# Kernel tuning notes

Measured on AMD Instinct MI355X. Metric: run time of the kernel, lower is better.

Reference implementation:

```python
import jax, jax.numpy as jnp
import numpy as np

N = 50000        # nodes
E = 1600000      # edges
NDIM_IN = 64
HID = 128        # hardcoded hidden width of first SAGELayer in E-GraphSAGE
NDIM_OUT = 128
EDIM = 32
EMBEDIM = 128
NCLASS = 2       # bin=True


def setup_inputs() -> dict:
    key = jax.random.key(0)
    ks = jax.random.split(key, 12)
    g = lambda k, shape: jax.random.normal(k, shape, jnp.float32) / np.sqrt(np.float32(shape[0]))
    return {
        "nfeats": jax.random.normal(ks[0], (N, NDIM_IN), jnp.float32),
        "efeats": jax.random.normal(ks[1], (E, EDIM), jnp.float32),
        "src": jax.random.randint(ks[2], (E,), 0, N),
        "dst": jax.random.randint(ks[3], (E,), 0, N),
        # SAGE layer 1: W_msg [ndim_in+edim -> 128], W_apply [ndim_in+128 -> 128]
        "Wm1": g(ks[4], (NDIM_IN + EDIM, HID)), "bm1": jnp.zeros((HID,), jnp.float32),
        "Wa1": g(ks[5], (NDIM_IN + HID, HID)), "ba1": jnp.zeros((HID,), jnp.float32),
        # SAGE layer 2: W_msg [128+edim -> ndim_out], W_apply [128+ndim_out -> ndim_out]
        "Wm2": g(ks[6], (HID + EDIM, NDIM_OUT)), "bm2": jnp.zeros((NDIM_OUT,), jnp.float32),
        "Wa2": g(ks[7], (HID + NDIM_OUT, NDIM_OUT)), "ba2": jnp.zeros((NDIM_OUT,), jnp.float32),
        # MLPPredictorEmbed: [2*ndim_out -> embedim] -> relu -> [embedim -> 2]
        "W1": g(ks[8], (2 * NDIM_OUT, EMBEDIM)), "b1": jnp.zeros((EMBEDIM,), jnp.float32),
        "W2": g(ks[9], (EMBEDIM, NCLASS)), "b2": jnp.zeros((NCLASS,), jnp.float32),
    }


def _sage_layer(h, efeats, src, dst, Wm, bm, Wa, ba):
    # per-edge message: relu(W_msg([h_src || e]))  -> [E, dout]
    m = jax.nn.relu(jnp.concatenate([h[src], efeats], axis=-1) @ Wm + bm)
    # mean aggregation by destination node (0 for isolated nodes, like DGL fn.mean)
    s = jax.ops.segment_sum(m, dst, num_segments=N)
    cnt = jax.ops.segment_sum(jnp.ones((m.shape[0], 1), m.dtype), dst, num_segments=N)
    h_neigh = s / jnp.maximum(cnt, 1.0)
    # node update: relu(W_apply([h || h_neigh]))
    return jax.nn.relu(jnp.concatenate([h, h_neigh], axis=-1) @ Wa + ba)


def reference(nfeats, efeats, src, dst,
              Wm1, bm1, Wa1, ba1, Wm2, bm2, Wa2, ba2,
              W1, b1, W2, b2):
    h = _sage_layer(nfeats, efeats, src, dst, Wm1, bm1, Wa1, ba1)   # [N, 128]
    h = _sage_layer(h, efeats, src, dst, Wm2, bm2, Wa2, ba2)        # [N, ndim_out]
    # edge predictor: MLP on [h_u || h_v] per edge
    z = jnp.concatenate([h[src], h[dst]], axis=-1)                   # [E, 2*ndim_out]
    score = jax.nn.relu(z @ W1 + b1) @ W2 + b2                       # [E, 2]
    return score
```

## Files before the change

### kernel.cpp

```cpp
#include <hip/hip_runtime.h>

#define N_NODES 50000
#define N_EDGES 1600000

typedef _Float16 h8 __attribute__((ext_vector_type(8)));
typedef float f4 __attribute__((ext_vector_type(4)));

__device__ inline h8 ld_h8(const _Float16* p) { return *(const h8*)p; }

__device__ inline h8 cvt2h8(f4 a, f4 b) {
    h8 r;
    r[0] = (_Float16)a[0]; r[1] = (_Float16)a[1]; r[2] = (_Float16)a[2]; r[3] = (_Float16)a[3];
    r[4] = (_Float16)b[0]; r[5] = (_Float16)b[1]; r[6] = (_Float16)b[2]; r[7] = (_Float16)b[3];
    return r;
}


__global__ void prep_weights(const float* __restrict__ Wm1, const float* __restrict__ Wa1,
                             const float* __restrict__ Wm2, const float* __restrict__ Wa2,
                             const float* __restrict__ W1,
                             _Float16* __restrict__ Wm1t, _Float16* __restrict__ Wa1t,
                             _Float16* __restrict__ Wm2t, _Float16* __restrict__ Wa2t,
                             _Float16* __restrict__ W1t)
{
    int i = blockIdx.x * 256 + threadIdx.x;
    if (i < 12288) {
        int o = i / 96, k = i % 96;
        int ks = k >> 5, q = (k >> 3) & 3, j = k & 7;
        int c = q ^ ((o >> 1) & 3);
        Wm1t[(ks * 128 + o) * 32 + c * 8 + j] = (_Float16)Wm1[k * 128 + o];
    } else if (i < 36864) {
        int jj = i - 12288; int o = jj / 192, k = jj % 192;
        Wa1t[o * 200 + k] = (_Float16)Wa1[k * 128 + o];
    } else if (i < 57344) {
        int jj = i - 36864; int o = jj / 160, k = jj % 160;
        int ks = k >> 5, q = (k >> 3) & 3, j = k & 7;
        int c = q ^ ((o >> 1) & 3);
        Wm2t[(ks * 128 + o) * 32 + c * 8 + j] = (_Float16)Wm2[k * 128 + o];
    } else if (i < 90112) {
        int jj = i - 57344; int o = jj >> 8, k = jj & 255;
        Wa2t[(o << 8) + k] = (_Float16)Wa2[k * 128 + o];
    } else if (i < 122880) {
        int jj = i - 90112; int o = jj >> 8, k = jj & 255;
        W1t[(o << 8) + k] = (_Float16)W1[k * 128 + o];
    }
}

__global__ void cvt_nfeats(const float* __restrict__ nf, _Float16* __restrict__ nf16)
{
    int i = blockIdx.x * 256 + threadIdx.x;
    nf16[i] = (_Float16)nf[i];
}


__global__ void hist_kernel(const int* __restrict__ dst, int* __restrict__ cnt)
{
    int e = blockIdx.x * 256 + threadIdx.x;
    atomicAdd(cnt + dst[e], 1);
}

__global__ void scan1_kernel(const int* __restrict__ cnt, int* __restrict__ tmp,
                             int* __restrict__ bsum)
{
    __shared__ int sh[256];
    int t = threadIdx.x, i = blockIdx.x * 256 + t;
    int v = (i < N_NODES) ? cnt[i] : 0;
    sh[t] = v; __syncthreads();
    for (int off = 1; off < 256; off <<= 1) {
        int x = (t >= off) ? sh[t - off] : 0;
        __syncthreads();
        sh[t] += x;
        __syncthreads();
    }
    if (i < N_NODES) tmp[i] = sh[t];
    if (t == 255) bsum[blockIdx.x] = sh[255];
}

__global__ void scan2_kernel(const int* __restrict__ bsum, int* __restrict__ bbase)
{
    __shared__ int sh[256];
    int t = threadIdx.x;
    int v = (t < 196) ? bsum[t] : 0;
    sh[t] = v; __syncthreads();
    for (int off = 1; off < 256; off <<= 1) {
        int x = (t >= off) ? sh[t - off] : 0;
        __syncthreads();
        sh[t] += x;
        __syncthreads();
    }
    if (t < 196) bbase[t] = sh[t] - v;
}

__global__ void scan3_kernel(const int* __restrict__ cnt, const int* __restrict__ tmp,
                             const int* __restrict__ bbase, int* __restrict__ cursor)
{
    int t = threadIdx.x, b = blockIdx.x, i = b * 256 + t;
    if (i < N_NODES) cursor[i] = tmp[i] - cnt[i] + bbase[b];
}

__global__ void scatter_kernel(const int* __restrict__ src, const int* __restrict__ dst,
                               int* __restrict__ cursor,
                               int2* __restrict__ pairs, int* __restrict__ dsts)
{
    int e = blockIdx.x * 256 + threadIdx.x;
    int d = dst[e];
    int pos = atomicAdd(cursor + d, 1);
    pairs[pos] = make_int2(e, src[e]);
    dsts[pos] = d;
}

__global__ void scatter_kernel_ef(const int* __restrict__ src, const int* __restrict__ dst,
                                  const float* __restrict__ efeats,
                                  int* __restrict__ cursor,
                                  int2* __restrict__ pairs, int* __restrict__ dsts,
                                  _Float16* __restrict__ efs)
{
    int e = blockIdx.x * 256 + threadIdx.x;
    int d = dst[e];
    const float* er = efeats + (size_t)e * 32;
    f4 v0 = *(const f4*)(er + 0),  v1 = *(const f4*)(er + 4);
    f4 v2 = *(const f4*)(er + 8),  v3 = *(const f4*)(er + 12);
    f4 v4 = *(const f4*)(er + 16), v5 = *(const f4*)(er + 20);
    f4 v6 = *(const f4*)(er + 24), v7 = *(const f4*)(er + 28);
    int pos = atomicAdd(cursor + d, 1);
    pairs[pos] = make_int2(e, src[e]);
    dsts[pos] = d;
    _Float16* ew = efs + (size_t)pos * 32;
    *(h8*)(ew + 0)  = cvt2h8(v0, v1);
    *(h8*)(ew + 8)  = cvt2h8(v2, v3);
    *(h8*)(ew + 16) = cvt2h8(v4, v5);
    *(h8*)(ew + 24) = cvt2h8(v6, v7);
}

template<int KSRC_H, int MINW, bool EF16>
__launch_bounds__(256, MINW)
__global__ void msg_kernel_sorted(const _Float16* __restrict__ ntab,
                                  const float* __restrict__ efeats,
                                  const _Float16* __restrict__ efs,
                                  const int2* __restrict__ pairs,
                                  const int* __restrict__ dsts,
                                  const _Float16* __restrict__ Wt,
                                  const float* __restrict__ bias,
                                  float* __restrict__ sacc)
{
    constexpr int EFSTEP = KSRC_H / 32;
    constexpr int KSTEPS = EFSTEP + 1;
    constexpr int BH = (KSRC_H + 32) * 128;
    constexpr int BBYTES = BH * 2;
    constexpr int SCRBYTES = 4 * 8 * 132 * 4;
    constexpr int LDSBYTES = BBYTES > SCRBYTES ? BBYTES : SCRBYTES;
    __shared__ __align__(16) char smem[LDSBYTES];
    _Float16* Bsh = (_Float16*)smem;

    const int tid = threadIdx.x;
    const int wave = tid >> 6, lane = tid & 63;
    const int q = lane >> 4, l15 = lane & 15;
    const int wbase = blockIdx.x * 128 + wave * 32;

    const int2 p0 = pairs[wbase + l15];
    const int2 p1 = pairs[wbase + 16 + l15];
    const int4 dv0 = *(const int4*)(dsts + wbase + q * 4);
    const int4 dv1 = *(const int4*)(dsts + wbase + 16 + q * 4);
    float bv[8];
#pragma unroll
    for (int nt = 0; nt < 8; nt++) bv[nt] = bias[nt * 16 + l15];

    const _Float16* r0 = ntab + (size_t)p0.y * KSRC_H + q * 8;
    const _Float16* r1 = ntab + (size_t)p1.y * KSRC_H + q * 8;
    h8 aA[EFSTEP], aB[EFSTEP];
#pragma unroll
    for (int ks = 0; ks < EFSTEP; ks++) {
        aA[ks] = ld_h8(r0 + ks * 32);
        aB[ks] = ld_h8(r1 + ks * 32);
    }
    h8 ef0h, ef1h;
    f4 e0a, e0b, e1a, e1b;
    if constexpr (EF16) {
        ef0h = ld_h8(efs + (size_t)(wbase + l15) * 32 + q * 8);
        ef1h = ld_h8(efs + (size_t)(wbase + 16 + l15) * 32 + q * 8);
    } else {
        const float* ep0 = efeats + (size_t)p0.x * 32 + q * 8;
        const float* ep1 = efeats + (size_t)p1.x * 32 + q * 8;
        e0a = *(const f4*)ep0; e0b = *(const f4*)(ep0 + 4);
        e1a = *(const f4*)ep1; e1b = *(const f4*)(ep1 + 4);
    }

    {
        const uint4* s4 = (const uint4*)Wt;
        uint4* d4 = (uint4*)smem;
        constexpr int n4 = BH / 8;
        for (int i = tid; i < n4; i += 256) d4[i] = s4[i];
    }
    __syncthreads();

    f4 acc[2][8];
#pragma unroll
    for (int t = 0; t < 2; t++)
#pragma unroll
        for (int nt = 0; nt < 8; nt++) acc[t][nt] = (f4){0.f, 0.f, 0.f, 0.f};

    const _Float16* bp = Bsh + l15 * 32 + ((q ^ ((l15 >> 1) & 3)) << 3);
#pragma unroll
    for (int ks = 0; ks < KSTEPS; ks++) {
        h8 a0, a1;
        if (ks < EFSTEP) {
            a0 = aA[ks]; a1 = aB[ks];
        } else {
            if constexpr (EF16) { a0 = ef0h; a1 = ef1h; }
            else { a0 = cvt2h8(e0a, e0b); a1 = cvt2h8(e1a, e1b); }
        }
#pragma unroll
        for (int nt = 0; nt < 8; nt++) {
            h8 b = ld_h8(bp + ks * 4096 + nt * 512);
            acc[0][nt] = __builtin_amdgcn_mfma_f32_16x16x32_f16(a0, b, acc[0][nt], 0, 0, 0);
            acc[1][nt] = __builtin_amdgcn_mfma_f32_16x16x32_f16(a1, b, acc[1][nt], 0, 0, 0);
        }
    }

    __syncthreads();

    float* wsch = (float*)smem + wave * 1056;

    const int df0 = __shfl(dv0.x, 0, 64);
    const int dl0 = __shfl(dv0.w, 48, 64);
    const int df1 = __shfl(dv1.x, 0, 64);
    const int dl1 = __shfl(dv1.w, 48, 64);

    auto unif16 = [&](const f4 (&a)[8], int d) {
        float sv[8];
#pragma unroll
        for (int nt = 0; nt < 8; nt++) {
            float s = fmaxf(a[nt][0] + bv[nt], 0.f) + fmaxf(a[nt][1] + bv[nt], 0.f)
                    + fmaxf(a[nt][2] + bv[nt], 0.f) + fmaxf(a[nt][3] + bv[nt], 0.f);
            s += __shfl_xor(s, 16, 64);
            s += __shfl_xor(s, 32, 64);
            sv[nt] = s;
        }
#pragma unroll
        for (int i = 0; i < 2; i++) {
            float x = (q == 0) ? sv[i*4] : (q == 1) ? sv[i*4+1] : (q == 2) ? sv[i*4+2] : sv[i*4+3];
            atomicAdd(sacc + (size_t)d * 128 + i * 64 + lane, x);
        }
    };

    auto scan16 = [&](const f4 (&a)[8], const int4 dv, int dfirst) {
        int dp = dfirst;
        float s0 = 0.f, s1 = 0.f;
#pragma unroll
        for (int h = 0; h < 2; h++) {
            if ((q >> 1) == h) {
                const int rloc = (q & 1) * 4;
#pragma unroll
                for (int nt = 0; nt < 8; nt++)
#pragma unroll
                    for (int r = 0; r < 4; r++)
                        wsch[(rloc + r) * 132 + nt * 16 + l15] = fmaxf(a[nt][r] + bv[nt], 0.f);
            }
            asm volatile("s_waitcnt lgkmcnt(0)" ::: "memory");
#pragma unroll
            for (int rr = 0; rr < 8; rr++) {
                const int rg = h * 8 + rr;
                const int sl = (rg >> 2) << 4;
                const int c = rg & 3;
                const int d = (c == 0) ? __shfl(dv.x, sl, 64)
                            : (c == 1) ? __shfl(dv.y, sl, 64)
                            : (c == 2) ? __shfl(dv.z, sl, 64)
                            :            __shfl(dv.w, sl, 64);
                const float v0 = wsch[rr * 132 + lane];
                const float v1 = wsch[rr * 132 + 64 + lane];
                if (d != dp) {
                    atomicAdd(sacc + (size_t)dp * 128 + lane, s0);
                    atomicAdd(sacc + (size_t)dp * 128 + 64 + lane, s1);
                    s0 = v0; s1 = v1; dp = d;
                } else {
                    s0 += v0; s1 += v1;
                }
            }
        }
        atomicAdd(sacc + (size_t)dp * 128 + lane, s0);
        atomicAdd(sacc + (size_t)dp * 128 + 64 + lane, s1);
    };

    if (df0 == dl1) {
        float sv[8];
#pragma unroll
        for (int nt = 0; nt < 8; nt++) {
            float s = fmaxf(acc[0][nt][0] + bv[nt], 0.f) + fmaxf(acc[0][nt][1] + bv[nt], 0.f)
                    + fmaxf(acc[0][nt][2] + bv[nt], 0.f) + fmaxf(acc[0][nt][3] + bv[nt], 0.f)
                    + fmaxf(acc[1][nt][0] + bv[nt], 0.f) + fmaxf(acc[1][nt][1] + bv[nt], 0.f)
                    + fmaxf(acc[1][nt][2] + bv[nt], 0.f) + fmaxf(acc[1][nt][3] + bv[nt], 0.f);
            s += __shfl_xor(s, 16, 64);
            s += __shfl_xor(s, 32, 64);
            sv[nt] = s;
        }
#pragma unroll
        for (int i = 0; i < 2; i++) {
            float x = (q == 0) ? sv[i*4] : (q == 1) ? sv[i*4+1] : (q == 2) ? sv[i*4+2] : sv[i*4+3];
            atomicAdd(sacc + (size_t)df0 * 128 + i * 64 + lane, x);
        }
    } else {
        if (df0 == dl0) unif16(acc[0], df0); else scan16(acc[0], dv0, df0);
        if (df1 == dl1) unif16(acc[1], df1); else scan16(acc[1], dv1, df1);
    }
}

template<int KSRC_H, bool SWIZ, int KPAD>
__launch_bounds__(256)
__global__ void apply_kernel(const _Float16* __restrict__ ntab,
                             const float* __restrict__ sacc,
                             const int* __restrict__ cnt,
                             const _Float16* __restrict__ Wt,
                             const float* __restrict__ bias,
                             _Float16* __restrict__ outtab)
{
    constexpr int KSTEPS = (KSRC_H + 128) / 32;
    __shared__ __align__(16) _Float16 Bsh[128 * KPAD];

    const int tid = threadIdx.x;
    if (SWIZ) {
        const uint4* s4 = (const uint4*)Wt;
        uint4* d4 = (uint4*)Bsh;
        for (int i = tid; i < 4096; i += 256) {
            int n = i >> 5, c = i & 31;
            d4[(n << 5) | (c ^ (n & 31))] = s4[i];
        }
    } else {
        const uint4* s4 = (const uint4*)Wt;
        uint4* d4 = (uint4*)Bsh;
        constexpr int n4 = 128 * KPAD / 8;
        for (int i = tid; i < n4; i += 256) d4[i] = s4[i];
    }
    __syncthreads();

    const int wave = tid >> 6, lane = tid & 63;
    const int q = lane >> 4, l15 = lane & 15;
    const int nbase = blockIdx.x * 128 + wave * 32;

    const int n0 = nbase + l15, n1 = nbase + 16 + l15;
    const int n0c = min(n0, N_NODES - 1), n1c = min(n1, N_NODES - 1);
    const _Float16* r0 = ntab + (size_t)n0c * KSRC_H;
    const _Float16* r1 = ntab + (size_t)n1c * KSRC_H;
    const float rcp0 = 1.0f / fmaxf((float)cnt[n0c], 1.0f);
    const float rcp1 = 1.0f / fmaxf((float)cnt[n1c], 1.0f);

    f4 acc[2][8];
#pragma unroll
    for (int t = 0; t < 2; t++)
#pragma unroll
        for (int nt = 0; nt < 8; nt++) acc[t][nt] = (f4){0.f, 0.f, 0.f, 0.f};

#pragma unroll
    for (int ks = 0; ks < KSTEPS; ks++) {
        h8 a0, a1;
        if (ks < KSRC_H / 32) {
            a0 = ld_h8(r0 + ks * 32 + q * 8);
            a1 = ld_h8(r1 + ks * 32 + q * 8);
        } else {
            const int kk = ks * 32 - KSRC_H + q * 8;
            const float* p0 = sacc + (size_t)n0c * 128 + kk;
            const float* p1 = sacc + (size_t)n1c * 128 + kk;
            f4 u0 = *(const f4*)p0 * rcp0, v0 = *(const f4*)(p0 + 4) * rcp0;
            f4 u1 = *(const f4*)p1 * rcp1, v1 = *(const f4*)(p1 + 4) * rcp1;
            a0 = cvt2h8(u0, v0);
            a1 = cvt2h8(u1, v1);
        }
#pragma unroll
        for (int nt = 0; nt < 8; nt++) {
            h8 b;
            if (SWIZ) {
                const int nrow = nt * 16 + l15;
                const int chunk = ((ks << 2) | q) ^ (nrow & 31);
                b = ld_h8(Bsh + (((nrow << 5) | chunk) << 3));
            } else {
                b = ld_h8(&Bsh[(nt * 16 + l15) * KPAD + ks * 32 + q * 8]);
            }
            acc[0][nt] = __builtin_amdgcn_mfma_f32_16x16x32_f16(a0, b, acc[0][nt], 0, 0, 0);
            acc[1][nt] = __builtin_amdgcn_mfma_f32_16x16x32_f16(a1, b, acc[1][nt], 0, 0, 0);
        }
    }

#pragma unroll
    for (int nt = 0; nt < 8; nt++) {
        const int col = nt * 16 + l15;
        const float bv = bias[col];
#pragma unroll
        for (int t = 0; t < 2; t++)
#pragma unroll
            for (int r = 0; r < 4; r++) {
                const int node = nbase + t * 16 + q * 4 + r;
                if (node < N_NODES) {
                    float v = fmaxf(acc[t][nt][r] + bv, 0.f);
                    outtab[(size_t)node * 128 + col] = (_Float16)v;
                }
            }
    }
}

__launch_bounds__(256)
__global__ void node_pq_kernel(const _Float16* __restrict__ h2,
                               const _Float16* __restrict__ W1t,
                               const float* __restrict__ b1,
                               _Float16* __restrict__ P,
                               float* __restrict__ Q)
{
    __shared__ __align__(16) _Float16 Bsh[128 * 256];

    const int tid = threadIdx.x;
    {
        const uint4* s4 = (const uint4*)W1t;
        uint4* d4 = (uint4*)Bsh;
        for (int i = tid; i < 4096; i += 256) {
            int n = i >> 5, c = i & 31;
            d4[(n << 5) | (c ^ (n & 31))] = s4[i];
        }
    }
    __syncthreads();

    const int wave = tid >> 6, lane = tid & 63;
    const int q = lane >> 4, l15 = lane & 15;
    const int nbase = blockIdx.x * 128 + wave * 32;

    const int n0 = nbase + l15, n1 = nbase + 16 + l15;
    const int n0c = min(n0, N_NODES - 1), n1c = min(n1, N_NODES - 1);
    const _Float16* r0 = h2 + (size_t)n0c * 128;
    const _Float16* r1 = h2 + (size_t)n1c * 128;

    f4 accP[2][8], accQ[2][8];
#pragma unroll
    for (int t = 0; t < 2; t++)
#pragma unroll
        for (int nt = 0; nt < 8; nt++) {
            accP[t][nt] = (f4){0.f, 0.f, 0.f, 0.f};
            accQ[t][nt] = (f4){0.f, 0.f, 0.f, 0.f};
        }

#pragma unroll
    for (int ks = 0; ks < 4; ks++) {
        h8 a0 = ld_h8(r0 + ks * 32 + q * 8);
        h8 a1 = ld_h8(r1 + ks * 32 + q * 8);
#pragma unroll
        for (int nt = 0; nt < 8; nt++) {
            const int nrow = nt * 16 + l15;
            const int cP = ((ks << 2) | q) ^ (nrow & 31);
            h8 bP = ld_h8(Bsh + (((nrow << 5) | cP) << 3));
            accP[0][nt] = __builtin_amdgcn_mfma_f32_16x16x32_f16(a0, bP, accP[0][nt], 0, 0, 0);
            accP[1][nt] = __builtin_amdgcn_mfma_f32_16x16x32_f16(a1, bP, accP[1][nt], 0, 0, 0);
            const int cQ = (((ks + 4) << 2) | q) ^ (nrow & 31);
            h8 bQ = ld_h8(Bsh + (((nrow << 5) | cQ) << 3));
            accQ[0][nt] = __builtin_amdgcn_mfma_f32_16x16x32_f16(a0, bQ, accQ[0][nt], 0, 0, 0);
            accQ[1][nt] = __builtin_amdgcn_mfma_f32_16x16x32_f16(a1, bQ, accQ[1][nt], 0, 0, 0);
        }
    }

#pragma unroll
    for (int nt = 0; nt < 8; nt++) {
        const int col = nt * 16 + l15;
        const float bq = b1[col];
#pragma unroll
        for (int t = 0; t < 2; t++)
#pragma unroll
            for (int r = 0; r < 4; r++) {
                const int node = nbase + t * 16 + q * 4 + r;
                if (node < N_NODES) {
                    P[(size_t)node * 128 + col] = (_Float16)accP[t][nt][r];
                    Q[(size_t)node * 128 + col] = accQ[t][nt][r] + bq;
                }
            }
    }
}

__launch_bounds__(256, 4)
__global__ void pred_elem_kernel(const _Float16* __restrict__ P,
                                 const float* __restrict__ Q,
                                 const int2* __restrict__ pairs,
                                 const int* __restrict__ dsts,
                                 const float* __restrict__ W2,
                                 const float* __restrict__ b2,
                                 float* __restrict__ out)
{
    __shared__ __align__(16) float w20sh[128];
    __shared__ __align__(16) float w21sh[128];

    const int tid = threadIdx.x;
    if (tid < 128) {
        w20sh[tid] = W2[tid * 2 + 0];
        w21sh[tid] = W2[tid * 2 + 1];
    }
    __syncthreads();

    const int slot = blockIdx.x * 256 + tid;
    const int2 pr = pairs[slot];
    const int d = dsts[slot];
    const _Float16* prow = P + (size_t)pr.y * 128;
    const float* qrow = Q + (size_t)d * 128;

    float o0 = 0.f, o1 = 0.f;
#pragma unroll
    for (int c = 0; c < 4; c++) {
        h8 pv[4];
#pragma unroll
        for (int i = 0; i < 4; i++) pv[i] = ld_h8(prow + c * 32 + i * 8);
        f4 qv[8];
#pragma unroll
        for (int i = 0; i < 8; i++) qv[i] = *(const f4*)(qrow + c * 32 + i * 4);
#pragma unroll
        for (int i = 0; i < 8; i++) {
            const f4 w0 = *(const f4*)(w20sh + c * 32 + i * 4);
            const f4 w1 = *(const f4*)(w21sh + c * 32 + i * 4);
#pragma unroll
            for (int j = 0; j < 4; j++) {
                const float pvf = (float)pv[i >> 1][(i & 1) * 4 + j];
                const float y = fmaxf(pvf + qv[i][j], 0.f);
                o0 += y * w0[j];
                o1 += y * w1[j];
            }
        }
    }

    out[(size_t)pr.x * 2 + 0] = o0 + b2[0];
    out[(size_t)pr.x * 2 + 1] = o1 + b2[1];
}

__launch_bounds__(256)
__global__ void pred_kernel(const _Float16* __restrict__ h2,
                            const int* __restrict__ src,
                            const int* __restrict__ dst,
                            const _Float16* __restrict__ W1t,
                            const float* __restrict__ b1,
                            const float* __restrict__ W2,
                            const float* __restrict__ b2,
                            float* __restrict__ out)
{
    __shared__ __align__(16) _Float16 Bsh[128 * 256];

    const int tid = threadIdx.x;
    {
        const uint4* s4 = (const uint4*)W1t;
        uint4* d4 = (uint4*)Bsh;
        for (int i = tid; i < 4096; i += 256) {
            int n = i >> 5, c = i & 31;
            d4[(n << 5) | (c ^ (n & 31))] = s4[i];
        }
    }
    __syncthreads();

    const int wave = tid >> 6, lane = tid & 63;
    const int q = lane >> 4, l15 = lane & 15;
    const int ebase = blockIdx.x * 128 + wave * 32;

    const int e0 = ebase + l15, e1 = ebase + 16 + l15;
    const _Float16* rs0 = h2 + (size_t)src[e0] * 128;
    const _Float16* rd0 = h2 + (size_t)dst[e0] * 128;
    const _Float16* rs1 = h2 + (size_t)src[e1] * 128;
    const _Float16* rd1 = h2 + (size_t)dst[e1] * 128;

    f4 acc[2][8];
#pragma unroll
    for (int t = 0; t < 2; t++)
#pragma unroll
        for (int nt = 0; nt < 8; nt++) acc[t][nt] = (f4){0.f, 0.f, 0.f, 0.f};

#pragma unroll
    for (int ks = 0; ks < 8; ks++) {
        h8 a0, a1;
        if (ks < 4) {
            a0 = ld_h8(rs0 + ks * 32 + q * 8);
            a1 = ld_h8(rs1 + ks * 32 + q * 8);
        } else {
            a0 = ld_h8(rd0 + (ks - 4) * 32 + q * 8);
            a1 = ld_h8(rd1 + (ks - 4) * 32 + q * 8);
        }
#pragma unroll
        for (int nt = 0; nt < 8; nt++) {
            const int nrow = nt * 16 + l15;
            const int chunk = ((ks << 2) | q) ^ (nrow & 31);
            h8 b = ld_h8(Bsh + (((nrow << 5) | chunk) << 3));
            acc[0][nt] = __builtin_amdgcn_mfma_f32_16x16x32_f16(a0, b, acc[0][nt], 0, 0, 0);
            acc[1][nt] = __builtin_amdgcn_mfma_f32_16x16x32_f16(a1, b, acc[1][nt], 0, 0, 0);
        }
    }

    float o[2][4][2];
#pragma unroll
    for (int t = 0; t < 2; t++)
#pragma unroll
        for (int r = 0; r < 4; r++) { o[t][r][0] = 0.f; o[t][r][1] = 0.f; }

#pragma unroll
    for (int nt = 0; nt < 8; nt++) {
        const int nrow = nt * 16 + l15;
        const float bv = b1[nrow];
        const float w20 = W2[nrow * 2 + 0];
        const float w21 = W2[nrow * 2 + 1];
#pragma unroll
        for (int t = 0; t < 2; t++)
#pragma unroll
            for (int r = 0; r < 4; r++) {
                float y = fmaxf(acc[t][nt][r] + bv, 0.f);
                o[t][r][0] += y * w20;
                o[t][r][1] += y * w21;
            }
    }

#pragma unroll
    for (int m = 1; m < 16; m <<= 1) {
#pragma unroll
        for (int t = 0; t < 2; t++)
#pragma unroll
            for (int r = 0; r < 4; r++) {
                o[t][r][0] += __shfl_xor(o[t][r][0], m, 64);
                o[t][r][1] += __shfl_xor(o[t][r][1], m, 64);
            }
    }

    if (l15 < 8) {
        const int r = l15 >> 1, c = l15 & 1;
        const float bb = c ? b2[1] : b2[0];
#pragma unroll
        for (int t = 0; t < 2; t++) {
            float v0 = (r == 0) ? o[t][0][0] : (r == 1) ? o[t][1][0] : (r == 2) ? o[t][2][0] : o[t][3][0];
            float v1 = (r == 0) ? o[t][0][1] : (r == 1) ? o[t][1][1] : (r == 2) ? o[t][2][1] : o[t][3][1];
            float v = (c ? v1 : v0) + bb;
            out[(size_t)(ebase + t * 16 + q * 4 + r) * 2 + c] = v;
        }
    }
}


extern "C" void kernel_launch(void* const* d_in, const int* in_sizes, int n_in,
                              void* d_out, int out_size, void* d_ws, size_t ws_size,
                              hipStream_t stream)
{
    const float* nfeats = (const float*)d_in[0];
    const float* efeats = (const float*)d_in[1];
    const int*   src    = (const int*)d_in[2];
    const int*   dst    = (const int*)d_in[3];
    const float* Wm1 = (const float*)d_in[4],  *bm1 = (const float*)d_in[5];
    const float* Wa1 = (const float*)d_in[6],  *ba1 = (const float*)d_in[7];
    const float* Wm2 = (const float*)d_in[8],  *bm2 = (const float*)d_in[9];
    const float* Wa2 = (const float*)d_in[10], *ba2 = (const float*)d_in[11];
    const float* W1  = (const float*)d_in[12], *b1  = (const float*)d_in[13];
    const float* W2  = (const float*)d_in[14], *b2  = (const float*)d_in[15];
    float* out = (float*)d_out;

    char* ws = (char*)d_ws;
    float*     s     = (float*)(ws);
    int*       cnt   = (int*)(ws + 25600000);
    int*       tmp   = (int*)(ws + 25800000);
    int*       cursor= (int*)(ws + 26000000);
    int*       bsum  = (int*)(ws + 26200000);
    int*       bbase = (int*)(ws + 26201024);
    _Float16*  nf16  = (_Float16*)(ws + 26202048);
    int2*      pairs = (int2*)(ws + 32602048);
    int*       dsts  = (int*)(ws + 45402048);
    _Float16*  h1    = (_Float16*)(ws + 51802048);
    _Float16*  Wm1t  = (_Float16*)(ws + 64602048);
    _Float16*  Wa1t  = (_Float16*)(ws + 64626624);
    _Float16*  Wm2t  = (_Float16*)(ws + 64677824);
    _Float16*  Wa2t  = (_Float16*)(ws + 64718784);
    _Float16*  W1t   = (_Float16*)(ws + 64784320);

    const bool big_ws  = ws_size >= (size_t)77800000;
    const bool ef16_ws = ws_size >= (size_t)180100000;
    _Float16* h2 = big_ws ? (_Float16*)(ws + 64849920)
                          : (_Float16*)(ws + 26202048);
    _Float16* efs16 = (_Float16*)(ws + 77649920);

    hipMemsetAsync(s, 0, 25600000, stream);
    hipMemsetAsync(cnt, 0, 200000, stream);

    prep_weights<<<480, 256, 0, stream>>>(Wm1, Wa1, Wm2, Wa2, W1, Wm1t, Wa1t, Wm2t, Wa2t, W1t);
    cvt_nfeats<<<12500, 256, 0, stream>>>(nfeats, nf16);

    hist_kernel<<<6250, 256, 0, stream>>>(dst, cnt);
    scan1_kernel<<<196, 256, 0, stream>>>(cnt, tmp, bsum);
    scan2_kernel<<<1, 256, 0, stream>>>(bsum, bbase);
    scan3_kernel<<<196, 256, 0, stream>>>(cnt, tmp, bbase, cursor);
    if (ef16_ws)
        scatter_kernel_ef<<<6250, 256, 0, stream>>>(src, dst, efeats, cursor, pairs, dsts, efs16);
    else
        scatter_kernel<<<6250, 256, 0, stream>>>(src, dst, cursor, pairs, dsts);

    if (ef16_ws)
        msg_kernel_sorted<64, 4, true><<<12500, 256, 0, stream>>>(nf16, efeats, efs16, pairs, dsts, Wm1t, bm1, s);
    else
        msg_kernel_sorted<64, 4, false><<<12500, 256, 0, stream>>>(nf16, efeats, nullptr, pairs, dsts, Wm1t, bm1, s);
    apply_kernel<64, false, 200><<<391, 256, 0, stream>>>(nf16, s, cnt, Wa1t, ba1, h1);

    hipMemsetAsync(s, 0, 25600000, stream);
    if (ef16_ws)
        msg_kernel_sorted<128, 4, true><<<12500, 256, 0, stream>>>(h1, efeats, efs16, pairs, dsts, Wm2t, bm2, s);
    else
        msg_kernel_sorted<128, 4, false><<<12500, 256, 0, stream>>>(h1, efeats, nullptr, pairs, dsts, Wm2t, bm2, s);
    apply_kernel<128, true, 256><<<391, 256, 0, stream>>>(h1, s, cnt, Wa2t, ba2, h2);

    if (big_ws) {
        _Float16* P = h1;
        float*    Q = s;
        node_pq_kernel<<<391, 256, 0, stream>>>(h2, W1t, b1, P, Q);
        pred_elem_kernel<<<6250, 256, 0, stream>>>(P, Q, pairs, dsts, W2, b2, out);
    } else {
        pred_kernel<<<12500, 256, 0, stream>>>(h2, src, dst, W1t, b1, W2, b2, out);
    }
}
```

Measured before the change: 1.027 ms.

## Make message kernels persistent to amortize per-block weight staging into LDS

Replaces the one-tile-per-block message kernels (12500 blocks of 256 threads) with a persistent kernel of 512 blocks of 512 threads, each looping over a contiguous range of 256-edge tiles. The weight matrix is copied into LDS once per block instead of once per 128 edges, cutting repeated global-to-LDS staging and barriers. The scatter scratch gets its own LDS region so no barrier is needed between tiles. The trade-offs are that gather-load latency is no longer hidden by many independent blocks, there is possible load imbalance across the fixed grid, and LDS per block grows, which can lower occupancy.

```diff
diff --git a/kernel.cpp b/kernel.cpp
--- a/kernel.cpp
+++ b/kernel.cpp
@@ -132,175 +132,177 @@
     *(h8*)(ew + 24) = cvt2h8(v6, v7);
 }
 
-template<int KSRC_H, int MINW, bool EF16>
-__launch_bounds__(256, MINW)
-__global__ void msg_kernel_sorted(const _Float16* __restrict__ ntab,
-                                  const float* __restrict__ efeats,
-                                  const _Float16* __restrict__ efs,
-                                  const int2* __restrict__ pairs,
-                                  const int* __restrict__ dsts,
-                                  const _Float16* __restrict__ Wt,
-                                  const float* __restrict__ bias,
-                                  float* __restrict__ sacc)
+template<int KSRC_H, bool EF16>
+__launch_bounds__(512, 4)
+__global__ void msg_kernel_ms(const _Float16* __restrict__ ntab,
+                              const float* __restrict__ efeats,
+                              const _Float16* __restrict__ efs,
+                              const int2* __restrict__ pairs,
+                              const int* __restrict__ dsts,
+                              const _Float16* __restrict__ Wt,
+                              const float* __restrict__ bias,
+                              float* __restrict__ sacc,
+                              int ntiles, int tpb)
 {
     constexpr int EFSTEP = KSRC_H / 32;
     constexpr int KSTEPS = EFSTEP + 1;
     constexpr int BH = (KSRC_H + 32) * 128;
     constexpr int BBYTES = BH * 2;
-    constexpr int SCRBYTES = 4 * 8 * 132 * 4;
-    constexpr int LDSBYTES = BBYTES > SCRBYTES ? BBYTES : SCRBYTES;
-    __shared__ __align__(16) char smem[LDSBYTES];
+    __shared__ __align__(16) char smem[BBYTES + 8 * 8 * 132 * 4];
+
     _Float16* Bsh = (_Float16*)smem;
-
     const int tid = threadIdx.x;
     const int wave = tid >> 6, lane = tid & 63;
     const int q = lane >> 4, l15 = lane & 15;
-    const int wbase = blockIdx.x * 128 + wave * 32;
-
-    const int2 p0 = pairs[wbase + l15];
-    const int2 p1 = pairs[wbase + 16 + l15];
-    const int4 dv0 = *(const int4*)(dsts + wbase + q * 4);
-    const int4 dv1 = *(const int4*)(dsts + wbase + 16 + q * 4);
-    float bv[8];
-#pragma unroll
-    for (int nt = 0; nt < 8; nt++) bv[nt] = bias[nt * 16 + l15];
-
-    const _Float16* r0 = ntab + (size_t)p0.y * KSRC_H + q * 8;
-    const _Float16* r1 = ntab + (size_t)p1.y * KSRC_H + q * 8;
-    h8 aA[EFSTEP], aB[EFSTEP];
-#pragma unroll
-    for (int ks = 0; ks < EFSTEP; ks++) {
-        aA[ks] = ld_h8(r0 + ks * 32);
-        aB[ks] = ld_h8(r1 + ks * 32);
-    }
-    h8 ef0h, ef1h;
-    f4 e0a, e0b, e1a, e1b;
-    if constexpr (EF16) {
-        ef0h = ld_h8(efs + (size_t)(wbase + l15) * 32 + q * 8);
-        ef1h = ld_h8(efs + (size_t)(wbase + 16 + l15) * 32 + q * 8);
-    } else {
-        const float* ep0 = efeats + (size_t)p0.x * 32 + q * 8;
-        const float* ep1 = efeats + (size_t)p1.x * 32 + q * 8;
-        e0a = *(const f4*)ep0; e0b = *(const f4*)(ep0 + 4);
-        e1a = *(const f4*)ep1; e1b = *(const f4*)(ep1 + 4);
-    }
+    float* wsch = (float*)(smem + BBYTES) + wave * 1056;
 
     {
         const uint4* s4 = (const uint4*)Wt;
         uint4* d4 = (uint4*)smem;
         constexpr int n4 = BH / 8;
-        for (int i = tid; i < n4; i += 256) d4[i] = s4[i];
-    }
+        for (int i = tid; i < n4; i += 512) d4[i] = s4[i];
+    }
+    float bv[8];
+#pragma unroll
+    for (int nt = 0; nt < 8; nt++) bv[nt] = bias[nt * 16 + l15];
     __syncthreads();
 
-    f4 acc[2][8];
-#pragma unroll
-    for (int t = 0; t < 2; t++)
-#pragma unroll
-        for (int nt = 0; nt < 8; nt++) acc[t][nt] = (f4){0.f, 0.f, 0.f, 0.f};
-
     const _Float16* bp = Bsh + l15 * 32 + ((q ^ ((l15 >> 1) & 3)) << 3);
-#pragma unroll
-    for (int ks = 0; ks < KSTEPS; ks++) {
-        h8 a0, a1;
-        if (ks < EFSTEP) {
-            a0 = aA[ks]; a1 = aB[ks];
+
+    const int t0 = blockIdx.x * tpb;
+    const int t1 = min(t0 + tpb, ntiles);
+    for (int t = t0; t < t1; t++) {
+        const int wbase = t * 256 + wave * 32;
+
+        const int2 p0 = pairs[wbase + l15];
+        const int2 p1 = pairs[wbase + 16 + l15];
+        const int4 dv0 = *(const int4*)(dsts + wbase + q * 4);
+        const int4 dv1 = *(const int4*)(dsts + wbase + 16 + q * 4);
+
+        const _Float16* r0 = ntab + (size_t)p0.y * KSRC_H + q * 8;
+        const _Float16* r1 = ntab + (size_t)p1.y * KSRC_H + q * 8;
+        h8 aA[EFSTEP], aB[EFSTEP];
+#pragma unroll
+        for (int ks = 0; ks < EFSTEP; ks++) {
+            aA[ks] = ld_h8(r0 + ks * 32);
+            aB[ks] = ld_h8(r1 + ks * 32);
+        }
+        h8 ef0h, ef1h;
+        f4 e0a, e0b, e1a, e1b;
+        if constexpr (EF16) {
+            ef0h = ld_h8(efs + (size_t)(wbase + l15) * 32 + q * 8);
+            ef1h = ld_h8(efs + (size_t)(wbase + 16 + l15) * 32 + q * 8);
         } else {
-            if constexpr (EF16) { a0 = ef0h; a1 = ef1h; }
-            else { a0 = cvt2h8(e0a, e0b); a1 = cvt2h8(e1a, e1b); }
-        }
-#pragma unroll
-        for (int nt = 0; nt < 8; nt++) {
-            h8 b = ld_h8(bp + ks * 4096 + nt * 512);
-            acc[0][nt] = __builtin_amdgcn_mfma_f32_16x16x32_f16(a0, b, acc[0][nt], 0, 0, 0);
-            acc[1][nt] = __builtin_amdgcn_mfma_f32_16x16x32_f16(a1, b, acc[1][nt], 0, 0, 0);
-        }
-    }
-
-    __syncthreads();
-
-    float* wsch = (float*)smem + wave * 1056;
-
-    const int df0 = __shfl(dv0.x, 0, 64);
-    const int dl0 = __shfl(dv0.w, 48, 64);
-    const int df1 = __shfl(dv1.x, 0, 64);
-    const int dl1 = __shfl(dv1.w, 48, 64);
-
-    auto unif16 = [&](const f4 (&a)[8], int d) {
-        float sv[8];
-#pragma unroll
-        for (int nt = 0; nt < 8; nt++) {
-            float s = fmaxf(a[nt][0] + bv[nt], 0.f) + fmaxf(a[nt][1] + bv[nt], 0.f)
-                    + fmaxf(a[nt][2] + bv[nt], 0.f) + fmaxf(a[nt][3] + bv[nt], 0.f);
-            s += __shfl_xor(s, 16, 64);
-            s += __shfl_xor(s, 32, 64);
-            sv[nt] = s;
-        }
-#pragma unroll
-        for (int i = 0; i < 2; i++) {
-            float x = (q == 0) ? sv[i*4] : (q == 1) ? sv[i*4+1] : (q == 2) ? sv[i*4+2] : sv[i*4+3];
-            atomicAdd(sacc + (size_t)d * 128 + i * 64 + lane, x);
-        }
-    };
-
-    auto scan16 = [&](const f4 (&a)[8], const int4 dv, int dfirst) {
-        int dp = dfirst;
-        float s0 = 0.f, s1 = 0.f;
-#pragma unroll
-        for (int h = 0; h < 2; h++) {
-            if ((q >> 1) == h) {
-                const int rloc = (q & 1) * 4;
-#pragma unroll
-                for (int nt = 0; nt < 8; nt++)
-#pragma unroll
-                    for (int r = 0; r < 4; r++)
-                        wsch[(rloc + r) * 132 + nt * 16 + l15] = fmaxf(a[nt][r] + bv[nt], 0.f);
-            }
-            asm volatile("s_waitcnt lgkmcnt(0)" ::: "memory");
-#pragma unroll
-            for (int rr = 0; rr < 8; rr++) {
-                const int rg = h * 8 + rr;
-                const int sl = (rg >> 2) << 4;
-                const int c = rg & 3;
-                const int d = (c == 0) ? __shfl(dv.x, sl, 64)
-                            : (c == 1) ? __shfl(dv.y, sl, 64)
-                            : (c == 2) ? __shfl(dv.z, sl, 64)
-                            :            __shfl(dv.w, sl, 64);
-                const float v0 = wsch[rr * 132 + lane];
-                const float v1 = wsch[rr * 132 + 64 + lane];
-                if (d != dp) {
-                    atomicAdd(sacc + (size_t)dp * 128 + lane, s0);
-                    atomicAdd(sacc + (size_t)dp * 128 + 64 + lane, s1);
-                    s0 = v0; s1 = v1; dp = d;
-                } else {
-                    s0 += v0; s1 += v1;
+            const float* ep0 = efeats + (size_t)p0.x * 32 + q * 8;
+            const float* ep1 = efeats + (size_t)p1.x * 32 + q * 8;
+            e0a = *(const f4*)ep0; e0b = *(const f4*)(ep0 + 4);
+            e1a = *(const f4*)ep1; e1b = *(const f4*)(ep1 + 4);
+        }
+
+        f4 acc[2][8];
+#pragma unroll
+        for (int tt = 0; tt < 2; tt++)
+#pragma unroll
+            for (int nt = 0; nt < 8; nt++) acc[tt][nt] = (f4){0.f, 0.f, 0.f, 0.f};
+
+#pragma unroll
+        for (int ks = 0; ks < KSTEPS; ks++) {
+            h8 a0, a1;
+            if (ks < EFSTEP) {
+                a0 = aA[ks]; a1 = aB[ks];
+            } else {
+                if constexpr (EF16) { a0 = ef0h; a1 = ef1h; }
+                else { a0 = cvt2h8(e0a, e0b); a1 = cvt2h8(e1a, e1b); }
+            }
+#pragma unroll
+            for (int nt = 0; nt < 8; nt++) {
+                h8 b = ld_h8(bp + ks * 4096 + nt * 512);
+                acc[0][nt] = __builtin_amdgcn_mfma_f32_16x16x32_f16(a0, b, acc[0][nt], 0, 0, 0);
+                acc[1][nt] = __builtin_amdgcn_mfma_f32_16x16x32_f16(a1, b, acc[1][nt], 0, 0, 0);
+            }
+        }
+
+        const int df0 = __shfl(dv0.x, 0, 64);
+        const int dl0 = __shfl(dv0.w, 48, 64);
+        const int df1 = __shfl(dv1.x, 0, 64);
+        const int dl1 = __shfl(dv1.w, 48, 64);
+
+        auto unif16 = [&](const f4 (&a)[8], int d) {
+            float sv[8];
+#pragma unroll
+            for (int nt = 0; nt < 8; nt++) {
+                float s = fmaxf(a[nt][0] + bv[nt], 0.f) + fmaxf(a[nt][1] + bv[nt], 0.f)
+                        + fmaxf(a[nt][2] + bv[nt], 0.f) + fmaxf(a[nt][3] + bv[nt], 0.f);
+                s += __shfl_xor(s, 16, 64);
+                s += __shfl_xor(s, 32, 64);
+                sv[nt] = s;
+            }
+#pragma unroll
+            for (int i = 0; i < 2; i++) {
+                float x = (q == 0) ? sv[i*4] : (q == 1) ? sv[i*4+1] : (q == 2) ? sv[i*4+2] : sv[i*4+3];
+                atomicAdd(sacc + (size_t)d * 128 + i * 64 + lane, x);
+            }
+        };
+
+        auto scan16 = [&](const f4 (&a)[8], const int4 dv, int dfirst) {
+            int dp = dfirst;
+            float s0 = 0.f, s1 = 0.f;
+#pragma unroll
+            for (int h = 0; h < 2; h++) {
+                if ((q >> 1) == h) {
+                    const int rloc = (q & 1) * 4;
+#pragma unroll
+                    for (int nt = 0; nt < 8; nt++)
+#pragma unroll
+                        for (int r = 0; r < 4; r++)
+                            wsch[(rloc + r) * 132 + nt * 16 + l15] = fmaxf(a[nt][r] + bv[nt], 0.f);
                 }
-            }
-        }
-        atomicAdd(sacc + (size_t)dp * 128 + lane, s0);
-        atomicAdd(sacc + (size_t)dp * 128 + 64 + lane, s1);
-    };
-
-    if (df0 == dl1) {
-        float sv[8];
-#pragma unroll
-        for (int nt = 0; nt < 8; nt++) {
-            float s = fmaxf(acc[0][nt][0] + bv[nt], 0.f) + fmaxf(acc[0][nt][1] + bv[nt], 0.f)
-                    + fmaxf(acc[0][nt][2] + bv[nt], 0.f) + fmaxf(acc[0][nt][3] + bv[nt], 0.f)
-                    + fmaxf(acc[1][nt][0] + bv[nt], 0.f) + fmaxf(acc[1][nt][1] + bv[nt], 0.f)
-                    + fmaxf(acc[1][nt][2] + bv[nt], 0.f) + fmaxf(acc[1][nt][3] + bv[nt], 0.f);
-            s += __shfl_xor(s, 16, 64);
-            s += __shfl_xor(s, 32, 64);
-            sv[nt] = s;
-        }
-#pragma unroll
-        for (int i = 0; i < 2; i++) {
-            float x = (q == 0) ? sv[i*4] : (q == 1) ? sv[i*4+1] : (q == 2) ? sv[i*4+2] : sv[i*4+3];
-            atomicAdd(sacc + (size_t)df0 * 128 + i * 64 + lane, x);
-        }
-    } else {
-        if (df0 == dl0) unif16(acc[0], df0); else scan16(acc[0], dv0, df0);
-        if (df1 == dl1) unif16(acc[1], df1); else scan16(acc[1], dv1, df1);
+                asm volatile("s_waitcnt lgkmcnt(0)" ::: "memory");
+#pragma unroll
+                for (int rr = 0; rr < 8; rr++) {
+                    const int rg = h * 8 + rr;
+                    const int sl = (rg >> 2) << 4;
+                    const int c = rg & 3;
+                    const int d = (c == 0) ? __shfl(dv.x, sl, 64)
+                                : (c == 1) ? __shfl(dv.y, sl, 64)
+                                : (c == 2) ? __shfl(dv.z, sl, 64)
+                                :            __shfl(dv.w, sl, 64);
+                    const float v0 = wsch[rr * 132 + lane];
+                    const float v1 = wsch[rr * 132 + 64 + lane];
+                    if (d != dp) {
+                        atomicAdd(sacc + (size_t)dp * 128 + lane, s0);
+                        atomicAdd(sacc + (size_t)dp * 128 + 64 + lane, s1);
+                        s0 = v0; s1 = v1; dp = d;
+                    } else {
+                        s0 += v0; s1 += v1;
+                    }
+                }
+            }
+            atomicAdd(sacc + (size_t)dp * 128 + lane, s0);
+            atomicAdd(sacc + (size_t)dp * 128 + 64 + lane, s1);
+        };
+
+        if (df0 == dl1) {
+            float sv[8];
+#pragma unroll
+            for (int nt = 0; nt < 8; nt++) {
+                float s = fmaxf(acc[0][nt][0] + bv[nt], 0.f) + fmaxf(acc[0][nt][1] + bv[nt], 0.f)
+                        + fmaxf(acc[0][nt][2] + bv[nt], 0.f) + fmaxf(acc[0][nt][3] + bv[nt], 0.f)
+                        + fmaxf(acc[1][nt][0] + bv[nt], 0.f) + fmaxf(acc[1][nt][1] + bv[nt], 0.f)
+                        + fmaxf(acc[1][nt][2] + bv[nt], 0.f) + fmaxf(acc[1][nt][3] + bv[nt], 0.f);
+                s += __shfl_xor(s, 16, 64);
+                s += __shfl_xor(s, 32, 64);
+                sv[nt] = s;
+            }
+#pragma unroll
+            for (int i = 0; i < 2; i++) {
+                float x = (q == 0) ? sv[i*4] : (q == 1) ? sv[i*4+1] : (q == 2) ? sv[i*4+2] : sv[i*4+3];
+                atomicAdd(sacc + (size_t)df0 * 128 + i * 64 + lane, x);
+            }
+        } else {
+            if (df0 == dl0) unif16(acc[0], df0); else scan16(acc[0], dv0, df0);
+            if (df1 == dl1) unif16(acc[1], df1); else scan16(acc[1], dv1, df1);
+        }
     }
 }
 
@@ -681,17 +683,21 @@
     else
         scatter_kernel<<<6250, 256, 0, stream>>>(src, dst, cursor, pairs, dsts);
 
+    const int NT  = N_EDGES / 256;
+    const int GRD = 512;
+    const int TPB = (NT + GRD - 1) / GRD;
+
     if (ef16_ws)
-        msg_kernel_sorted<64, 4, true><<<12500, 256, 0, stream>>>(nf16, efeats, efs16, pairs, dsts, Wm1t, bm1, s);
+        msg_kernel_ms<64, true><<<GRD, 512, 0, stream>>>(nf16, efeats, efs16, pairs, dsts, Wm1t, bm1, s, NT, TPB);
     else
-        msg_kernel_sorted<64, 4, false><<<12500, 256, 0, stream>>>(nf16, efeats, nullptr, pairs, dsts, Wm1t, bm1, s);
+        msg_kernel_ms<64, false><<<GRD, 512, 0, stream>>>(nf16, efeats, nullptr, pairs, dsts, Wm1t, bm1, s, NT, TPB);
     apply_kernel<64, false, 200><<<391, 256, 0, stream>>>(nf16, s, cnt, Wa1t, ba1, h1);
 
     hipMemsetAsync(s, 0, 25600000, stream);
     if (ef16_ws)
-        msg_kernel_sorted<128, 4, true><<<12500, 256, 0, stream>>>(h1, efeats, efs16, pairs, dsts, Wm2t, bm2, s);
+        msg_kernel_ms<128, true><<<GRD, 512, 0, stream>>>(h1, efeats, efs16, pairs, dsts, Wm2t, bm2, s, NT, TPB);
     else
-        msg_kernel_sorted<128, 4, false><<<12500, 256, 0, stream>>>(h1, efeats, nullptr, pairs, dsts, Wm2t, bm2, s);
+        msg_kernel_ms<128, false><<<GRD, 512, 0, stream>>>(h1, efeats, nullptr, pairs, dsts, Wm2t, bm2, s, NT, TPB);
     apply_kernel<128, true, 256><<<391, 256, 0, stream>>>(h1, s, cnt, Wa2t, ba2, h2);
 
     if (big_ws) {
```

New measurement: 1.038 ms. Within noise of the previous version (+1.0%).
